# Kernel tuning notes

Measured on AMD Instinct MI355X. Metric: run time of the kernel, lower is better.

Reference implementation:

```python
import jax, jax.numpy as jnp
import numpy as np

SPLINE_ORDER = 3
TOP_K = 2
NUM_EXPERTS = 8


def _gram_basis(x, beta_w):
    # x: (B, C, H, W) post-tanh. Returns (B, C*(S+1), H, W).
    P0 = jnp.ones_like(x)
    P1 = x
    ps = [P0, P1]
    for i in range(2, SPLINE_ORDER + 1):
        n, m = i - 1, i
        # beta(n, m) = (m+n)*(m-n)*n^2 / (m^2/(4n^2-1)) * beta_weights[n]
        beta = (m + n) * (m - n) * (n ** 2) * (4.0 * n ** 2 - 1.0) / (m ** 2) * beta_w[n]
        P2 = x * ps[-1] - beta * ps[-2]
        ps.append(P2)
    return jnp.concatenate(ps, axis=1)


def _expert(x, poly_w, beta_w):
    # tanh -> Gram polynomial basis -> SiLU -> conv2d (padding=1, stride=1)
    g = jax.nn.silu(_gram_basis(jnp.tanh(x), beta_w))
    return jax.lax.conv_general_dilated(
        g, poly_w[0], window_strides=(1, 1), padding=[(1, 1), (1, 1)],
        dimension_numbers=('NCHW', 'OIHW', 'NCHW'))


def _cv_squared(v):
    # torch.var is unbiased (ddof=1)
    return jnp.var(v, ddof=1) / (jnp.mean(v) ** 2 + 1e-10)


def reference(x, w_gate, poly_weights, beta_weights):
    B = x.shape[0]
    # gating input: global average pool -> (B, C)
    gate_x = jnp.mean(x, axis=(2, 3))
    probs = jax.nn.softmax(gate_x @ w_gate, axis=1)  # softmax BEFORE topk, as in source
    top_vals, top_idx = jax.lax.top_k(probs, TOP_K + 1)
    tk_vals = top_vals[:, :TOP_K]
    tk_idx = top_idx[:, :TOP_K]
    tk_gates = tk_vals / (jnp.sum(tk_vals, axis=1, keepdims=True) + 1e-6)
    gates = jnp.zeros_like(probs).at[jnp.arange(B)[:, None], tk_idx].set(tk_gates)
    importance = gates.sum(axis=0)
    load = jnp.sum(gates > 0, axis=0).astype(jnp.float32)  # eval-mode load
    loss = (_cv_squared(importance) + _cv_squared(load)) * 0.01
    # All experts share parameters (ModuleList([experts]*num_experts)), so
    # sum_e gates[b,e] * expert_e(x[b]) == gates.sum(1)[b] * expert(x[b]).
    y = _expert(x, poly_weights, beta_weights) * jnp.sum(gates, axis=1)[:, None, None, None]
    return y, loss


def setup_inputs() -> dict:
    key = jax.random.key(0)
    k1, k2, k3, k4 = jax.random.split(key, 4)
    x = jax.random.normal(k1, (16, 32, 192, 192), dtype=jnp.float32)
    w_gate = jax.random.normal(k2, (32, NUM_EXPERTS), dtype=jnp.float32) * 0.1
    poly_weights = jax.random.normal(k3, (1, 32, 32 * (SPLINE_ORDER + 1), 3, 3), dtype=jnp.float32) * 0.05
    beta_weights = jax.random.normal(k4, (SPLINE_ORDER + 1,), dtype=jnp.float32) * 0.01
    return {"x": x, "w_gate": w_gate, "poly_weights": poly_weights, "beta_weights": beta_weights}
```

## Files before the change

kernel.cpp:

```cpp
#include <hip/hip_runtime.h>

typedef unsigned short u16;
typedef unsigned int u32;
typedef __attribute__((ext_vector_type(8))) short bf16x8;
typedef __attribute__((ext_vector_type(4))) float f32x4;

static constexpr int B = 16, C = 32, H = 192, W = 192;
static constexpr int HW = H * W;
static constexpr int E = 8;
static constexpr int CO = 32;
static constexpr int NB = 96;
static constexpr long long NTOT = (long long)B * C * HW;
static constexpr float SILU1 = 0.7310585786300049f;

static constexpr size_t GP_OFF  = (size_t)NTOT * 2;
static constexpr size_t SCL_OFF = GP_OFF + (size_t)B * C * NB * 4;
static constexpr size_t SK_OFF  = SCL_OFF + 128;
static constexpr size_t SS_OFF  = SK_OFF + 288 * 4;
static constexpr size_t WF_OFF  = SS_OFF + 128;

__device__ inline u16 f2b(float f) {
    u32 u = __float_as_uint(f);
    return (u16)((u + 0x7fffu + ((u >> 16) & 1u)) >> 16);
}
__device__ inline float silu(float z) { return z / (1.0f + __expf(-z)); }
__device__ inline float tanh_fast(float z) {
    float e = __expf(2.0f * z);
    return 1.0f - 2.0f * __builtin_amdgcn_rcpf(e + 1.0f);
}

__global__ __launch_bounds__(256) void stage1_prep(const float* __restrict__ x,
                                                   const float* __restrict__ pw,
                                                   u16* __restrict__ t_out,
                                                   float* __restrict__ gpart,
                                                   float* __restrict__ Sk,
                                                   float* __restrict__ Ssum,
                                                   u16* __restrict__ wfrag) {
    __shared__ float sg[2][4][16];
    __shared__ float sred[9][32][8];
    __shared__ float sks[288];
    const int blk = blockIdx.x, tid = threadIdx.x;
    if (blk < B * NB) {
        const int b = blk / NB, band = blk - (blk / NB) * NB;
        const int cp = tid & 15, part = tid >> 4;
        const size_t pbase = (size_t)b * HW + (size_t)(band * 2) * W;
        const float4* xa = (const float4*)(x + (size_t)(b * C + 2 * cp) * HW
                                             + (size_t)(band * 2) * W);
        const float4* xb = (const float4*)(x + (size_t)(b * C + 2 * cp + 1) * HW
                                             + (size_t)(band * 2) * W);
        u32* tw = (u32*)t_out;
        float s0 = 0.0f, s1 = 0.0f;
        #pragma unroll
        for (int k = 0; k < 6; ++k) {
            const int j = k * 16 + part;
            float4 a = xa[j], c = xb[j];
            s0 += (a.x + a.y) + (a.z + a.w);
            s1 += (c.x + c.y) + (c.z + c.w);
            u32 r0 = (u32)f2b(tanh_fast(a.x)) | ((u32)f2b(tanh_fast(c.x)) << 16);
            u32 r1 = (u32)f2b(tanh_fast(a.y)) | ((u32)f2b(tanh_fast(c.y)) << 16);
            u32 r2 = (u32)f2b(tanh_fast(a.z)) | ((u32)f2b(tanh_fast(c.z)) << 16);
            u32 r3 = (u32)f2b(tanh_fast(a.w)) | ((u32)f2b(tanh_fast(c.w)) << 16);
            u32* dst = tw + (pbase + (size_t)j * 4) * 16 + cp;
            dst[0] = r0; dst[16] = r1; dst[32] = r2; dst[48] = r3;
        }
        s0 += __shfl_down(s0, 32); s0 += __shfl_down(s0, 16);
        s1 += __shfl_down(s1, 32); s1 += __shfl_down(s1, 16);
        if ((part & 3) == 0) { sg[0][tid >> 6][cp] = s0; sg[1][tid >> 6][cp] = s1; }
        __syncthreads();
        if (tid < 32) {
            const int cpp = tid >> 1, o = tid & 1;
            gpart[(size_t)(b * C + tid) * NB + band] =
                (sg[o][0][cpp] + sg[o][1][cpp]) + (sg[o][2][cpp] + sg[o][3][cpp]);
        }
        return;
    }
    if (blk < B * NB + 108) {
        int j = (blk - B * NB) * 256 + tid;
        int e = j & 7, lane = (j >> 3) & 63, rest = j >> 9;
        int half = rest & 1, pt = rest >> 1;
        int p = pt / 9, tap = pt - p * 9;
        int co = half * 16 + (lane & 15);
        int ci = 32 + p * 32 + (lane >> 4) * 8 + e;
        wfrag[j] = f2b(pw[(size_t)co * 1152 + ci * 9 + tap]);
        return;
    }
    {
        const int co = tid & 31, sub = tid >> 5;
        #pragma unroll
        for (int k = 0; k < 9; ++k) {
            float s = 0.0f;
            #pragma unroll
            for (int i = 0; i < 4; ++i)
                s += pw[(size_t)co * 1152 + (sub * 4 + i) * 9 + k];
            sred[k][co][sub] = s;
        }
        __syncthreads();
        for (int j = tid; j < 288; j += 256) {
            int k = j >> 5, c = j & 31;
            float s = 0.0f;
            #pragma unroll
            for (int u = 0; u < 8; ++u) s += sred[k][c][u];
            sks[j] = s; Sk[j] = s;
        }
        __syncthreads();
        if (tid < 32) {
            float s = 0.0f;
            #pragma unroll
            for (int k = 0; k < 9; ++k) s += sks[k * 32 + tid];
            Ssum[tid] = s;
        }
    }
}

__global__ __launch_bounds__(512) void gate_k(const float* __restrict__ gpart,
                                              const float* __restrict__ wg,
                                              float* __restrict__ scl,
                                              float* __restrict__ out) {
    __shared__ float gx[B][C];
    __shared__ float lg[B][E];
    __shared__ float gt[B][E];
    const int tid = threadIdx.x;
    {
        const float4* gp = (const float4*)(gpart + (size_t)tid * NB);
        float s = 0.0f;
        #pragma unroll
        for (int k = 0; k < NB / 4; ++k) { float4 v = gp[k]; s += (v.x + v.y) + (v.z + v.w); }
        gx[tid >> 5][tid & 31] = s * (1.0f / HW);
    }
    __syncthreads();
    if (tid < B * E) {
        const int gb = tid >> 3, ge = tid & 7;
        float s = 0.0f;
        #pragma unroll
        for (int c = 0; c < C; ++c) s += gx[gb][c] * wg[c * E + ge];
        lg[gb][ge] = s;
    }
    __syncthreads();
    if (tid < B) {
        float p[E];
        float m = lg[tid][0];
        #pragma unroll
        for (int e = 1; e < E; ++e) m = fmaxf(m, lg[tid][e]);
        float sum = 0.0f;
        #pragma unroll
        for (int e = 0; e < E; ++e) { p[e] = __expf(lg[tid][e] - m); sum += p[e]; }
        float inv = 1.0f / sum;
        #pragma unroll
        for (int e = 0; e < E; ++e) p[e] *= inv;
        int i0 = 0; float v0g = p[0];
        #pragma unroll
        for (int e = 1; e < E; ++e) if (p[e] > v0g) { v0g = p[e]; i0 = e; }
        int i1 = -1; float v1g = -1.0f;
        #pragma unroll
        for (int e = 0; e < E; ++e) { if (e == i0) continue; if (p[e] > v1g) { v1g = p[e]; i1 = e; } }
        const float denom = v0g + v1g + 1e-6f;
        #pragma unroll
        for (int e = 0; e < E; ++e) gt[tid][e] = 0.0f;
        gt[tid][i0] = v0g / denom; gt[tid][i1] = v1g / denom;
        scl[tid] = gt[tid][i0] + gt[tid][i1];
    }
    __syncthreads();
    if (tid == 0) {
        float imp[E], ld[E];
        #pragma unroll
        for (int e = 0; e < E; ++e) { imp[e] = 0.0f; ld[e] = 0.0f; }
        for (int bb = 0; bb < B; ++bb)
            #pragma unroll
            for (int e = 0; e < E; ++e) {
                float g = gt[bb][e];
                imp[e] += g;
                if (g > 0.0f) ld[e] += 1.0f;
            }
        float mi = 0.0f, mld = 0.0f;
        #pragma unroll
        for (int e = 0; e < E; ++e) { mi += imp[e]; mld += ld[e]; }
        mi *= (1.0f / E); mld *= (1.0f / E);
        float vi = 0.0f, vl = 0.0f;
        #pragma unroll
        for (int e = 0; e < E; ++e) {
            float di = imp[e] - mi, dl = ld[e] - mld;
            vi += di * di; vl += dl * dl;
        }
        vi *= (1.0f / (E - 1)); vl *= (1.0f / (E - 1));
        out[NTOT] = (vi / (mi * mi + 1e-10f) + vl / (mld * mld + 1e-10f)) * 0.01f;
    }
}

static constexpr int GSTR = 40;

__global__ __launch_bounds__(256) void conv_mfma(const u16* __restrict__ t_ws,
                                                 const u16* __restrict__ wfrag,
                                                 const float* __restrict__ beta_w,
                                                 const float* __restrict__ scl_ws,
                                                 const float* __restrict__ Sk,
                                                 const float* __restrict__ Ssum,
                                                 float* __restrict__ out) {
    __shared__ __align__(16) u16 gtile[324 * GSTR];

    const int b = blockIdx.z;
    const int gx0 = blockIdx.x << 4, gy0 = blockIdx.y << 4;
    const int tid = threadIdx.x;
    const int w = tid >> 6, lane = tid & 63, q = lane >> 4, ml = lane & 15;
    const float beta2 = 2.25f * beta_w[1];
    const float beta23 = beta2 + (300.0f / 9.0f) * beta_w[2];

    const int p0 = tid;
    int extra = -1;
    if ((tid & 3) == 0) extra = tid >> 2;
    else if ((tid & 63) == 1) extra = 64 + (tid >> 6);
    const int p1 = (extra >= 0) ? 256 + extra : -1;

    u32 pk0[16], pk1[16];
    bool v0, v1 = false;
    {
        int py = p0 / 18, px = p0 - py * 18;
        int gy = gy0 + py - 1, gx = gx0 + px - 1;
        v0 = (unsigned)gy < (unsigned)H && (unsigned)gx < (unsigned)W;
        if (v0) {
            const uint4* tp = (const uint4*)(t_ws + (((size_t)b * HW + (size_t)gy * W + gx) << 5));
            *(uint4*)&pk0[0]  = tp[0];
            *(uint4*)&pk0[4]  = tp[1];
            *(uint4*)&pk0[8]  = tp[2];
            *(uint4*)&pk0[12] = tp[3];
        } else {
            #pragma unroll
            for (int cc = 0; cc < 16; ++cc) pk0[cc] = 0u;
        }
        if (p1 >= 0) {
            int py1 = p1 / 18, px1 = p1 - py1 * 18;
            int gy1 = gy0 + py1 - 1, gx1 = gx0 + px1 - 1;
            v1 = (unsigned)gy1 < (unsigned)H && (unsigned)gx1 < (unsigned)W;
            if (v1) {
                const uint4* tp = (const uint4*)(t_ws + (((size_t)b * HW + (size_t)gy1 * W + gx1) << 5));
                *(uint4*)&pk1[0]  = tp[0];
                *(uint4*)&pk1[4]  = tp[1];
                *(uint4*)&pk1[8]  = tp[2];
                *(uint4*)&pk1[12] = tp[3];
            }
        }
        if (!v1) {
            #pragma unroll
            for (int cc = 0; cc < 16; ++cc) pk1[cc] = 0u;
        }
    }

    const float sc = scl_ws[b];

    f32x4 acc[4][2];
    #pragma unroll
    for (int a = 0; a < 4; ++a) {
        acc[a][0] = (f32x4){0.0f, 0.0f, 0.0f, 0.0f};
        acc[a][1] = (f32x4){0.0f, 0.0f, 0.0f, 0.0f};
    }

    #pragma unroll
    for (int p = 0; p < 3; ++p) {
        if (p) __syncthreads();
        #pragma unroll
        for (int slot = 0; slot < 2; ++slot) {
            const int pix = slot ? p1 : p0;
            if (slot && p1 < 0) continue;
            const bool vv = slot ? v1 : v0;
            const u32* pk = slot ? pk1 : pk0;
            u32 r[16];
            if (vv) {
                #pragma unroll
                for (int cc = 0; cc < 16; ++cc) {
                    float tl = __uint_as_float(pk[cc] << 16);
                    float th = __uint_as_float(pk[cc] & 0xffff0000u);
                    float ul, uh;
                    if (p == 0) { ul = tl; uh = th; }
                    else if (p == 1) { ul = fmaf(tl, tl, -beta2); uh = fmaf(th, th, -beta2); }
                    else { ul = tl * fmaf(tl, tl, -beta23); uh = th * fmaf(th, th, -beta23); }
                    u32 gl = __float_as_uint(silu(ul)) + 0x8000u;
                    u32 gh = __float_as_uint(silu(uh)) + 0x8000u;
                    r[cc] = (gl >> 16) | (gh & 0xffff0000u);
                }
            } else {
                #pragma unroll
                for (int cc = 0; cc < 16; ++cc) r[cc] = 0u;
            }
            uint4* dst = (uint4*)&gtile[pix * GSTR];
            dst[0] = *(const uint4*)&r[0];
            dst[1] = *(const uint4*)&r[4];
            dst[2] = *(const uint4*)&r[8];
            dst[3] = *(const uint4*)&r[12];
        }
        __syncthreads();
        const u16* wf = wfrag + (size_t)p * 9216;
        #pragma unroll
        for (int dx = 0; dx < 3; ++dx) {
            bf16x8 bf[3][2];
            #pragma unroll
            for (int dyi = 0; dyi < 3; ++dyi) {
                const int tap = dyi * 3 + dx;
                bf[dyi][0] = *(const bf16x8*)(wf + ((size_t)(tap * 2 + 0) * 64 + lane) * 8);
                bf[dyi][1] = *(const bf16x8*)(wf + ((size_t)(tap * 2 + 1) * 64 + lane) * 8);
            }
            #pragma unroll
            for (int rl = 0; rl < 6; ++rl) {
                const bf16x8 af = *(const bf16x8*)
                    &gtile[(((w << 2) + rl) * 18 + ml + dx) * GSTR + (q << 3)];
                #pragma unroll
                for (int dyi = 0; dyi < 3; ++dyi) {
                    const int a = rl - dyi;
                    if (a >= 0 && a < 4) {
                        acc[a][0] = __builtin_amdgcn_mfma_f32_16x16x32_bf16(af, bf[dyi][0], acc[a][0], 0, 0, 0);
                        acc[a][1] = __builtin_amdgcn_mfma_f32_16x16x32_bf16(af, bf[dyi][1], acc[a][1], 0, 0, 0);
                    }
                }
            }
        }
    }

    const bool interior = (blockIdx.x > 0) && (blockIdx.x < 11) &&
                          (blockIdx.y > 0) && (blockIdx.y < 11);
    #pragma unroll
    for (int half = 0; half < 2; ++half) {
        const int co = half * 16 + ml;
        const float bfull = SILU1 * Ssum[co];
        #pragma unroll
        for (int a = 0; a < 4; ++a) {
            const int y = gy0 + (w << 2) + a;
            float ov[4];
            #pragma unroll
            for (int r = 0; r < 4; ++r) {
                float bias = bfull;
                if (!interior) {
                    const int xg = gx0 + (q << 2) + r;
                    bias = 0.0f;
                    #pragma unroll
                    for (int k = 0; k < 9; ++k) {
                        int yy = y + k / 3 - 1, xx = xg + k % 3 - 1;
                        if ((unsigned)yy < (unsigned)H && (unsigned)xx < (unsigned)W)
                            bias += Sk[k * 32 + co];
                    }
                    bias *= SILU1;
                }
                ov[r] = (acc[a][half][r] + bias) * sc;
            }
            *(float4*)&out[((size_t)(b * CO + co) * H + y) * W + gx0 + (q << 2)] = *(float4*)ov;
        }
    }
}

extern "C" void kernel_launch(void* const* d_in, const int* in_sizes, int n_in,
                              void* d_out, int out_size, void* d_ws, size_t ws_size,
                              hipStream_t stream) {
    const float* x  = (const float*)d_in[0];
    const float* wg = (const float*)d_in[1];
    const float* pw = (const float*)d_in[2];
    const float* bw = (const float*)d_in[3];
    float* out = (float*)d_out;
    char* ws = (char*)d_ws;
    u16*   t_ws  = (u16*)ws;
    float* gpart = (float*)(ws + GP_OFF);
    float* scl   = (float*)(ws + SCL_OFF);
    float* Sk    = (float*)(ws + SK_OFF);
    float* Ssum  = (float*)(ws + SS_OFF);
    u16*   wfrag = (u16*)(ws + WF_OFF);

    stage1_prep<<<dim3(B * NB + 109), 256, 0, stream>>>(x, pw, t_ws, gpart, Sk, Ssum, wfrag);
    gate_k<<<dim3(1), 512, 0, stream>>>(gpart, wg, scl, out);
    conv_mfma<<<dim3(12, 12, B), 256, 0, stream>>>(t_ws, wfrag, bw, scl, Sk, Ssum, out);
}
```

Measured before the change: 267.2 us.

## Precompute SiLU Gram basis in prep kernel and double-buffer conv loads

Moves the SiLU(Gram polynomial) evaluation out of the conv kernel into the prep pass. The prep pass now writes three bf16 basis planes per pixel (96 channels) instead of one tanh plane. The conv kernel then just streams the precomputed planes into LDS, prefetching the next phase's plane into registers while MFMAs run on the current one. This avoids redoing the transcendental work for halo pixels across overlapping tiles, and it overlaps global loads with compute. The cost is three times the intermediate workspace write and read traffic, plus more registers held for the prefetch buffers.

```diff
diff --git a/kernel.cpp b/kernel.cpp
--- a/kernel.cpp
+++ b/kernel.cpp
@@ -13,7 +13,8 @@
 static constexpr long long NTOT = (long long)B * C * HW;
 static constexpr float SILU1 = 0.7310585786300049f;
 
-static constexpr size_t GP_OFF  = (size_t)NTOT * 2;
+static constexpr size_t G_BYTES = (size_t)B * HW * 192;
+static constexpr size_t GP_OFF  = G_BYTES;
 static constexpr size_t SCL_OFF = GP_OFF + (size_t)B * C * NB * 4;
 static constexpr size_t SK_OFF  = SCL_OFF + 128;
 static constexpr size_t SS_OFF  = SK_OFF + 288 * 4;
@@ -31,7 +32,8 @@
 
 __global__ __launch_bounds__(256) void stage1_prep(const float* __restrict__ x,
                                                    const float* __restrict__ pw,
-                                                   u16* __restrict__ t_out,
+                                                   const float* __restrict__ beta_w,
+                                                   u16* __restrict__ g_out,
                                                    float* __restrict__ gpart,
                                                    float* __restrict__ Sk,
                                                    float* __restrict__ Ssum,
@@ -43,12 +45,14 @@
     if (blk < B * NB) {
         const int b = blk / NB, band = blk - (blk / NB) * NB;
         const int cp = tid & 15, part = tid >> 4;
+        const float beta2 = 2.25f * beta_w[1];
+        const float beta23 = beta2 + (300.0f / 9.0f) * beta_w[2];
         const size_t pbase = (size_t)b * HW + (size_t)(band * 2) * W;
         const float4* xa = (const float4*)(x + (size_t)(b * C + 2 * cp) * HW
                                              + (size_t)(band * 2) * W);
         const float4* xb = (const float4*)(x + (size_t)(b * C + 2 * cp + 1) * HW
                                              + (size_t)(band * 2) * W);
-        u32* tw = (u32*)t_out;
+        u32* tw = (u32*)g_out;
         float s0 = 0.0f, s1 = 0.0f;
         #pragma unroll
         for (int k = 0; k < 6; ++k) {
@@ -56,12 +60,22 @@
             float4 a = xa[j], c = xb[j];
             s0 += (a.x + a.y) + (a.z + a.w);
             s1 += (c.x + c.y) + (c.z + c.w);
-            u32 r0 = (u32)f2b(tanh_fast(a.x)) | ((u32)f2b(tanh_fast(c.x)) << 16);
-            u32 r1 = (u32)f2b(tanh_fast(a.y)) | ((u32)f2b(tanh_fast(c.y)) << 16);
-            u32 r2 = (u32)f2b(tanh_fast(a.z)) | ((u32)f2b(tanh_fast(c.z)) << 16);
-            u32 r3 = (u32)f2b(tanh_fast(a.w)) | ((u32)f2b(tanh_fast(c.w)) << 16);
-            u32* dst = tw + (pbase + (size_t)j * 4) * 16 + cp;
-            dst[0] = r0; dst[16] = r1; dst[32] = r2; dst[48] = r3;
+            u32* dst = tw + (pbase + (size_t)j * 4) * 48 + cp;
+            const float av[4] = {a.x, a.y, a.z, a.w};
+            const float cv[4] = {c.x, c.y, c.z, c.w};
+            #pragma unroll
+            for (int n = 0; n < 4; ++n) {
+                const float ta = tanh_fast(av[n]), tc = tanh_fast(cv[n]);
+                u32 w1 = (u32)f2b(silu(ta)) | ((u32)f2b(silu(tc)) << 16);
+                const float qa = fmaf(ta, ta, -beta2), qc = fmaf(tc, tc, -beta2);
+                u32 w2 = (u32)f2b(silu(qa)) | ((u32)f2b(silu(qc)) << 16);
+                const float ra = ta * fmaf(ta, ta, -beta23);
+                const float rc = tc * fmaf(tc, tc, -beta23);
+                u32 w3 = (u32)f2b(silu(ra)) | ((u32)f2b(silu(rc)) << 16);
+                dst[n * 48]      = w1;
+                dst[n * 48 + 16] = w2;
+                dst[n * 48 + 32] = w3;
+            }
         }
         s0 += __shfl_down(s0, 32); s0 += __shfl_down(s0, 16);
         s1 += __shfl_down(s1, 32); s1 += __shfl_down(s1, 16);
@@ -188,9 +202,8 @@
 
 static constexpr int GSTR = 40;
 
-__global__ __launch_bounds__(256) void conv_mfma(const u16* __restrict__ t_ws,
+__global__ __launch_bounds__(256) void conv_mfma(const u16* __restrict__ g_ws,
                                                  const u16* __restrict__ wfrag,
-                                                 const float* __restrict__ beta_w,
                                                  const float* __restrict__ scl_ws,
                                                  const float* __restrict__ Sk,
                                                  const float* __restrict__ Ssum,
@@ -201,8 +214,6 @@
     const int gx0 = blockIdx.x << 4, gy0 = blockIdx.y << 4;
     const int tid = threadIdx.x;
     const int w = tid >> 6, lane = tid & 63, q = lane >> 4, ml = lane & 15;
-    const float beta2 = 2.25f * beta_w[1];
-    const float beta23 = beta2 + (300.0f / 9.0f) * beta_w[2];
 
     const int p0 = tid;
     int extra = -1;
@@ -210,41 +221,53 @@
     else if ((tid & 63) == 1) extra = 64 + (tid >> 6);
     const int p1 = (extra >= 0) ? 256 + extra : -1;
 
-    u32 pk0[16], pk1[16];
-    bool v0, v1 = false;
+    const u32* gsrc = (const u32*)g_ws;
+    size_t base0 = 0, base1 = 0;
+    bool v0 = false, v1 = false;
     {
         int py = p0 / 18, px = p0 - py * 18;
         int gy = gy0 + py - 1, gx = gx0 + px - 1;
         v0 = (unsigned)gy < (unsigned)H && (unsigned)gx < (unsigned)W;
-        if (v0) {
-            const uint4* tp = (const uint4*)(t_ws + (((size_t)b * HW + (size_t)gy * W + gx) << 5));
-            *(uint4*)&pk0[0]  = tp[0];
-            *(uint4*)&pk0[4]  = tp[1];
-            *(uint4*)&pk0[8]  = tp[2];
-            *(uint4*)&pk0[12] = tp[3];
-        } else {
-            #pragma unroll
-            for (int cc = 0; cc < 16; ++cc) pk0[cc] = 0u;
-        }
+        if (v0) base0 = ((size_t)b * HW + (size_t)gy * W + gx) * 48;
         if (p1 >= 0) {
             int py1 = p1 / 18, px1 = p1 - py1 * 18;
             int gy1 = gy0 + py1 - 1, gx1 = gx0 + px1 - 1;
             v1 = (unsigned)gy1 < (unsigned)H && (unsigned)gx1 < (unsigned)W;
-            if (v1) {
-                const uint4* tp = (const uint4*)(t_ws + (((size_t)b * HW + (size_t)gy1 * W + gx1) << 5));
-                *(uint4*)&pk1[0]  = tp[0];
-                *(uint4*)&pk1[4]  = tp[1];
-                *(uint4*)&pk1[8]  = tp[2];
-                *(uint4*)&pk1[12] = tp[3];
-            }
-        }
-        if (!v1) {
-            #pragma unroll
-            for (int cc = 0; cc < 16; ++cc) pk1[cc] = 0u;
+            if (v1) base1 = ((size_t)b * HW + (size_t)gy1 * W + gx1) * 48;
         }
     }
 
     const float sc = scl_ws[b];
+
+    u32 rA0[16], rA1[16], rB0[16], rB1[16];
+    #pragma unroll
+    for (int i = 0; i < 16; ++i) { rA0[i] = 0u; rA1[i] = 0u; rB0[i] = 0u; rB1[i] = 0u; }
+
+#define LOADC(P, R0, R1)                                                        \
+    do {                                                                        \
+        if (v0) {                                                               \
+            const uint4* tp = (const uint4*)(gsrc + base0 + (P) * 16);          \
+            *(uint4*)&R0[0] = tp[0]; *(uint4*)&R0[4]  = tp[1];                  \
+            *(uint4*)&R0[8] = tp[2]; *(uint4*)&R0[12] = tp[3];                  \
+        }                                                                       \
+        if (p1 >= 0 && v1) {                                                    \
+            const uint4* tp = (const uint4*)(gsrc + base1 + (P) * 16);          \
+            *(uint4*)&R1[0] = tp[0]; *(uint4*)&R1[4]  = tp[1];                  \
+            *(uint4*)&R1[8] = tp[2]; *(uint4*)&R1[12] = tp[3];                  \
+        }                                                                       \
+    } while (0)
+
+#define STORE_LDS(R0, R1)                                                       \
+    do {                                                                        \
+        uint4* d0 = (uint4*)&gtile[p0 * GSTR];                                  \
+        d0[0] = *(uint4*)&R0[0]; d0[1] = *(uint4*)&R0[4];                       \
+        d0[2] = *(uint4*)&R0[8]; d0[3] = *(uint4*)&R0[12];                      \
+        if (p1 >= 0) {                                                          \
+            uint4* d1 = (uint4*)&gtile[p1 * GSTR];                              \
+            d1[0] = *(uint4*)&R1[0]; d1[1] = *(uint4*)&R1[4];                   \
+            d1[2] = *(uint4*)&R1[8]; d1[3] = *(uint4*)&R1[12];                  \
+        }                                                                       \
+    } while (0)
 
     f32x4 acc[4][2];
     #pragma unroll
@@ -253,65 +276,55 @@
         acc[a][1] = (f32x4){0.0f, 0.0f, 0.0f, 0.0f};
     }
 
-    #pragma unroll
-    for (int p = 0; p < 3; ++p) {
-        if (p) __syncthreads();
-        #pragma unroll
-        for (int slot = 0; slot < 2; ++slot) {
-            const int pix = slot ? p1 : p0;
-            if (slot && p1 < 0) continue;
-            const bool vv = slot ? v1 : v0;
-            const u32* pk = slot ? pk1 : pk0;
-            u32 r[16];
-            if (vv) {
-                #pragma unroll
-                for (int cc = 0; cc < 16; ++cc) {
-                    float tl = __uint_as_float(pk[cc] << 16);
-                    float th = __uint_as_float(pk[cc] & 0xffff0000u);
-                    float ul, uh;
-                    if (p == 0) { ul = tl; uh = th; }
-                    else if (p == 1) { ul = fmaf(tl, tl, -beta2); uh = fmaf(th, th, -beta2); }
-                    else { ul = tl * fmaf(tl, tl, -beta23); uh = th * fmaf(th, th, -beta23); }
-                    u32 gl = __float_as_uint(silu(ul)) + 0x8000u;
-                    u32 gh = __float_as_uint(silu(uh)) + 0x8000u;
-                    r[cc] = (gl >> 16) | (gh & 0xffff0000u);
-                }
-            } else {
-                #pragma unroll
-                for (int cc = 0; cc < 16; ++cc) r[cc] = 0u;
-            }
-            uint4* dst = (uint4*)&gtile[pix * GSTR];
-            dst[0] = *(const uint4*)&r[0];
-            dst[1] = *(const uint4*)&r[4];
-            dst[2] = *(const uint4*)&r[8];
-            dst[3] = *(const uint4*)&r[12];
-        }
-        __syncthreads();
-        const u16* wf = wfrag + (size_t)p * 9216;
-        #pragma unroll
-        for (int dx = 0; dx < 3; ++dx) {
-            bf16x8 bf[3][2];
-            #pragma unroll
-            for (int dyi = 0; dyi < 3; ++dyi) {
-                const int tap = dyi * 3 + dx;
-                bf[dyi][0] = *(const bf16x8*)(wf + ((size_t)(tap * 2 + 0) * 64 + lane) * 8);
-                bf[dyi][1] = *(const bf16x8*)(wf + ((size_t)(tap * 2 + 1) * 64 + lane) * 8);
-            }
-            #pragma unroll
-            for (int rl = 0; rl < 6; ++rl) {
-                const bf16x8 af = *(const bf16x8*)
-                    &gtile[(((w << 2) + rl) * 18 + ml + dx) * GSTR + (q << 3)];
-                #pragma unroll
-                for (int dyi = 0; dyi < 3; ++dyi) {
-                    const int a = rl - dyi;
-                    if (a >= 0 && a < 4) {
-                        acc[a][0] = __builtin_amdgcn_mfma_f32_16x16x32_bf16(af, bf[dyi][0], acc[a][0], 0, 0, 0);
-                        acc[a][1] = __builtin_amdgcn_mfma_f32_16x16x32_bf16(af, bf[dyi][1], acc[a][1], 0, 0, 0);
-                    }
-                }
-            }
-        }
-    }
+#define MFMA_PHASE(P)                                                           \
+    do {                                                                        \
+        const u16* wf = wfrag + (size_t)(P) * 9216;                             \
+        _Pragma("unroll")                                                       \
+        for (int dx = 0; dx < 3; ++dx) {                                        \
+            bf16x8 bf[3][2];                                                    \
+            _Pragma("unroll")                                                   \
+            for (int dyi = 0; dyi < 3; ++dyi) {                                 \
+                const int tap = dyi * 3 + dx;                                   \
+                bf[dyi][0] = *(const bf16x8*)(wf + ((size_t)(tap * 2 + 0) * 64 + lane) * 8); \
+                bf[dyi][1] = *(const bf16x8*)(wf + ((size_t)(tap * 2 + 1) * 64 + lane) * 8); \
+            }                                                                   \
+            _Pragma("unroll")                                                   \
+            for (int rl = 0; rl < 6; ++rl) {                                    \
+                const bf16x8 af = *(const bf16x8*)                              \
+                    &gtile[(((w << 2) + rl) * 18 + ml + dx) * GSTR + (q << 3)]; \
+                _Pragma("unroll")                                               \
+                for (int dyi = 0; dyi < 3; ++dyi) {                             \
+                    const int a = rl - dyi;                                     \
+                    if (a >= 0 && a < 4) {                                      \
+                        acc[a][0] = __builtin_amdgcn_mfma_f32_16x16x32_bf16(af, bf[dyi][0], acc[a][0], 0, 0, 0); \
+                        acc[a][1] = __builtin_amdgcn_mfma_f32_16x16x32_bf16(af, bf[dyi][1], acc[a][1], 0, 0, 0); \
+                    }                                                           \
+                }                                                               \
+            }                                                                   \
+        }                                                                       \
+    } while (0)
+
+    LOADC(0, rA0, rA1);
+
+    STORE_LDS(rA0, rA1);
+    LOADC(1, rB0, rB1);
+    __syncthreads();
+    MFMA_PHASE(0);
+    __syncthreads();
+
+    STORE_LDS(rB0, rB1);
+    LOADC(2, rA0, rA1);
+    __syncthreads();
+    MFMA_PHASE(1);
+    __syncthreads();
+
+    STORE_LDS(rA0, rA1);
+    __syncthreads();
+    MFMA_PHASE(2);
+
+#undef LOADC
+#undef STORE_LDS
+#undef MFMA_PHASE
 
     const bool interior = (blockIdx.x > 0) && (blockIdx.x < 11) &&
                           (blockIdx.y > 0) && (blockIdx.y < 11);
@@ -353,14 +366,14 @@
     const float* bw = (const float*)d_in[3];
     float* out = (float*)d_out;
     char* ws = (char*)d_ws;
-    u16*   t_ws  = (u16*)ws;
+    u16*   g_ws  = (u16*)ws;
     float* gpart = (float*)(ws + GP_OFF);
     float* scl   = (float*)(ws + SCL_OFF);
     float* Sk    = (float*)(ws + SK_OFF);
     float* Ssum  = (float*)(ws + SS_OFF);
     u16*   wfrag = (u16*)(ws + WF_OFF);
 
-    stage1_prep<<<dim3(B * NB + 109), 256, 0, stream>>>(x, pw, t_ws, gpart, Sk, Ssum, wfrag);
+    stage1_prep<<<dim3(B * NB + 109), 256, 0, stream>>>(x, pw, bw, g_ws, gpart, Sk, Ssum, wfrag);
     gate_k<<<dim3(1), 512, 0, stream>>>(gpart, wg, scl, out);
-    conv_mfma<<<dim3(12, 12, B), 256, 0, stream>>>(t_ws, wfrag, bw, scl, Sk, Ssum, out);
-}
+    conv_mfma<<<dim3(12, 12, B), 256, 0, stream>>>(g_ws, wfrag, scl, Sk, Ssum, out);
+}
```

Measured after the change: 289.4 us. +8.3%, slower.

## Double-buffer basis tile to drop a barrier and use packed bf16 conversion

Applied to the files above, without the earlier changes.

The conv kernel now keeps two LDS buffers for the Gram basis tile and alternates them across the three polynomial phases. This removes one __syncthreads per phase and lets basis computation for the next phase overlap with MFMA work still running on the previous buffer. SiLU now multiplies by a hardware reciprocal instead of dividing. Float-to-bf16 packing in both kernels uses the v_cvt_pk_bf16_f32 instruction in place of manual bit manipulation. LDS use doubles, which may reduce occupancy, and the approximate reciprocal and packed conversion can change rounding slightly.

```diff
diff --git a/kernel.cpp b/kernel.cpp
--- a/kernel.cpp
+++ b/kernel.cpp
@@ -19,11 +19,18 @@
 static constexpr size_t SS_OFF  = SK_OFF + 288 * 4;
 static constexpr size_t WF_OFF  = SS_OFF + 128;
 
+__device__ inline u32 cvt_pk_bf16(float lo, float hi) {
+    u32 r;
+    asm("v_cvt_pk_bf16_f32 %0, %1, %2" : "=v"(r) : "v"(lo), "v"(hi));
+    return r;
+}
 __device__ inline u16 f2b(float f) {
     u32 u = __float_as_uint(f);
     return (u16)((u + 0x7fffu + ((u >> 16) & 1u)) >> 16);
 }
-__device__ inline float silu(float z) { return z / (1.0f + __expf(-z)); }
+__device__ inline float silu_fast(float z) {
+    return z * __builtin_amdgcn_rcpf(1.0f + __expf(-z));
+}
 __device__ inline float tanh_fast(float z) {
     float e = __expf(2.0f * z);
     return 1.0f - 2.0f * __builtin_amdgcn_rcpf(e + 1.0f);
@@ -56,10 +63,10 @@
             float4 a = xa[j], c = xb[j];
             s0 += (a.x + a.y) + (a.z + a.w);
             s1 += (c.x + c.y) + (c.z + c.w);
-            u32 r0 = (u32)f2b(tanh_fast(a.x)) | ((u32)f2b(tanh_fast(c.x)) << 16);
-            u32 r1 = (u32)f2b(tanh_fast(a.y)) | ((u32)f2b(tanh_fast(c.y)) << 16);
-            u32 r2 = (u32)f2b(tanh_fast(a.z)) | ((u32)f2b(tanh_fast(c.z)) << 16);
-            u32 r3 = (u32)f2b(tanh_fast(a.w)) | ((u32)f2b(tanh_fast(c.w)) << 16);
+            u32 r0 = cvt_pk_bf16(tanh_fast(a.x), tanh_fast(c.x));
+            u32 r1 = cvt_pk_bf16(tanh_fast(a.y), tanh_fast(c.y));
+            u32 r2 = cvt_pk_bf16(tanh_fast(a.z), tanh_fast(c.z));
+            u32 r3 = cvt_pk_bf16(tanh_fast(a.w), tanh_fast(c.w));
             u32* dst = tw + (pbase + (size_t)j * 4) * 16 + cp;
             dst[0] = r0; dst[16] = r1; dst[32] = r2; dst[48] = r3;
         }
@@ -195,7 +202,7 @@
                                                  const float* __restrict__ Sk,
                                                  const float* __restrict__ Ssum,
                                                  float* __restrict__ out) {
-    __shared__ __align__(16) u16 gtile[324 * GSTR];
+    __shared__ __align__(16) u16 gtile[2][324 * GSTR];
 
     const int b = blockIdx.z;
     const int gx0 = blockIdx.x << 4, gy0 = blockIdx.y << 4;
@@ -246,6 +253,38 @@
 
     const float sc = scl_ws[b];
 
+#define BASIS(P, BUF)                                                           \
+    do {                                                                        \
+        _Pragma("unroll")                                                       \
+        for (int slot = 0; slot < 2; ++slot) {                                  \
+            const int pix = slot ? p1 : p0;                                     \
+            if (slot && p1 < 0) continue;                                       \
+            const bool vv = slot ? v1 : v0;                                     \
+            const u32* pk = slot ? pk1 : pk0;                                   \
+            u32 r[16];                                                          \
+            if (vv) {                                                           \
+                _Pragma("unroll")                                               \
+                for (int cc = 0; cc < 16; ++cc) {                               \
+                    float tl = __uint_as_float(pk[cc] << 16);                   \
+                    float th = __uint_as_float(pk[cc] & 0xffff0000u);           \
+                    float ul, uh;                                               \
+                    if ((P) == 0) { ul = tl; uh = th; }                         \
+                    else if ((P) == 1) { ul = fmaf(tl, tl, -beta2); uh = fmaf(th, th, -beta2); } \
+                    else { ul = tl * fmaf(tl, tl, -beta23); uh = th * fmaf(th, th, -beta23); } \
+                    r[cc] = cvt_pk_bf16(silu_fast(ul), silu_fast(uh));          \
+                }                                                               \
+            } else {                                                            \
+                _Pragma("unroll")                                               \
+                for (int cc = 0; cc < 16; ++cc) r[cc] = 0u;                     \
+            }                                                                   \
+            uint4* dst = (uint4*)&gtile[BUF][pix * GSTR];                       \
+            dst[0] = *(const uint4*)&r[0];                                      \
+            dst[1] = *(const uint4*)&r[4];                                      \
+            dst[2] = *(const uint4*)&r[8];                                      \
+            dst[3] = *(const uint4*)&r[12];                                     \
+        }                                                                       \
+    } while (0)
+
     f32x4 acc[4][2];
     #pragma unroll
     for (int a = 0; a < 4; ++a) {
@@ -253,65 +292,46 @@
         acc[a][1] = (f32x4){0.0f, 0.0f, 0.0f, 0.0f};
     }
 
-    #pragma unroll
-    for (int p = 0; p < 3; ++p) {
-        if (p) __syncthreads();
-        #pragma unroll
-        for (int slot = 0; slot < 2; ++slot) {
-            const int pix = slot ? p1 : p0;
-            if (slot && p1 < 0) continue;
-            const bool vv = slot ? v1 : v0;
-            const u32* pk = slot ? pk1 : pk0;
-            u32 r[16];
-            if (vv) {
-                #pragma unroll
-                for (int cc = 0; cc < 16; ++cc) {
-                    float tl = __uint_as_float(pk[cc] << 16);
-                    float th = __uint_as_float(pk[cc] & 0xffff0000u);
-                    float ul, uh;
-                    if (p == 0) { ul = tl; uh = th; }
-                    else if (p == 1) { ul = fmaf(tl, tl, -beta2); uh = fmaf(th, th, -beta2); }
-                    else { ul = tl * fmaf(tl, tl, -beta23); uh = th * fmaf(th, th, -beta23); }
-                    u32 gl = __float_as_uint(silu(ul)) + 0x8000u;
-                    u32 gh = __float_as_uint(silu(uh)) + 0x8000u;
-                    r[cc] = (gl >> 16) | (gh & 0xffff0000u);
-                }
-            } else {
-                #pragma unroll
-                for (int cc = 0; cc < 16; ++cc) r[cc] = 0u;
-            }
-            uint4* dst = (uint4*)&gtile[pix * GSTR];
-            dst[0] = *(const uint4*)&r[0];
-            dst[1] = *(const uint4*)&r[4];
-            dst[2] = *(const uint4*)&r[8];
-            dst[3] = *(const uint4*)&r[12];
-        }
-        __syncthreads();
-        const u16* wf = wfrag + (size_t)p * 9216;
-        #pragma unroll
-        for (int dx = 0; dx < 3; ++dx) {
-            bf16x8 bf[3][2];
-            #pragma unroll
-            for (int dyi = 0; dyi < 3; ++dyi) {
-                const int tap = dyi * 3 + dx;
-                bf[dyi][0] = *(const bf16x8*)(wf + ((size_t)(tap * 2 + 0) * 64 + lane) * 8);
-                bf[dyi][1] = *(const bf16x8*)(wf + ((size_t)(tap * 2 + 1) * 64 + lane) * 8);
-            }
-            #pragma unroll
-            for (int rl = 0; rl < 6; ++rl) {
-                const bf16x8 af = *(const bf16x8*)
-                    &gtile[(((w << 2) + rl) * 18 + ml + dx) * GSTR + (q << 3)];
-                #pragma unroll
-                for (int dyi = 0; dyi < 3; ++dyi) {
-                    const int a = rl - dyi;
-                    if (a >= 0 && a < 4) {
-                        acc[a][0] = __builtin_amdgcn_mfma_f32_16x16x32_bf16(af, bf[dyi][0], acc[a][0], 0, 0, 0);
-                        acc[a][1] = __builtin_amdgcn_mfma_f32_16x16x32_bf16(af, bf[dyi][1], acc[a][1], 0, 0, 0);
-                    }
-                }
-            }
-        }
-    }
+#define MFMA_PHASE(P, BUF)                                                      \
+    do {                                                                        \
+        const u16* wf = wfrag + (size_t)(P) * 9216;                             \
+        _Pragma("unroll")                                                       \
+        for (int dx = 0; dx < 3; ++dx) {                                        \
+            bf16x8 bf[3][2];                                                    \
+            _Pragma("unroll")                                                   \
+            for (int dyi = 0; dyi < 3; ++dyi) {                                 \
+                const int tap = dyi * 3 + dx;                                   \
+                bf[dyi][0] = *(const bf16x8*)(wf + ((size_t)(tap * 2 + 0) * 64 + lane) * 8); \
+                bf[dyi][1] = *(const bf16x8*)(wf + ((size_t)(tap * 2 + 1) * 64 + lane) * 8); \
+            }                                                                   \
+            _Pragma("unroll")                                                   \
+            for (int rl = 0; rl < 6; ++rl) {                                    \
+                const bf16x8 af = *(const bf16x8*)                              \
+                    &gtile[BUF][(((w << 2) + rl) * 18 + ml + dx) * GSTR + (q << 3)]; \
+                _Pragma("unroll")                                               \
+                for (int dyi = 0; dyi < 3; ++dyi) {                             \
+                    const int a = rl - dyi;                                     \
+                    if (a >= 0 && a < 4) {                                      \
+                        acc[a][0] = __builtin_amdgcn_mfma_f32_16x16x32_bf16(af, bf[dyi][0], acc[a][0], 0, 0, 0); \
+                        acc[a][1] = __builtin_amdgcn_mfma_f32_16x16x32_bf16(af, bf[dyi][1], acc[a][1], 0, 0, 0); \
+                    }                                                           \
+                }                                                               \
+            }                                                                   \
+        }                                                                       \
+    } while (0)
+
+    BASIS(0, 0);
+    __syncthreads();
+    MFMA_PHASE(0, 0);
+    BASIS(1, 1);
+    __syncthreads();
+    MFMA_PHASE(1, 1);
+    BASIS(2, 0);
+    __syncthreads();
+    MFMA_PHASE(2, 0);
+
+#undef BASIS
+#undef MFMA_PHASE
 
     const bool interior = (blockIdx.x > 0) && (blockIdx.x < 11) &&
                           (blockIdx.y > 0) && (blockIdx.y < 11);
```

Result: faster. 245.8 us (-8.0%).
